# Kernel optimization log

Measured on AMD Instinct MI355X. Metric: run time of the kernel, lower is better.

## Reference

```python
import jax, jax.numpy as jnp
import numpy as np

B, L, H, NH = 8, 256, 128, 4
D = H // NH
NEG = jnp.float32(-(2.0 ** 32) + 1.0)


def setup_inputs() -> dict:
    key = jax.random.key(0)
    ks = jax.random.split(key, 12)
    f = lambda k, s, sc=1.0: jax.random.normal(k, s, dtype=jnp.float32) * sc
    inp = {
        "queries": f(ks[0], (B, L, H)),
        "keys": f(ks[1], (B, L, H)),
        "time_matrix_K": f(ks[2], (B, L, L, H), 0.05),
        "time_matrix_V": f(ks[3], (B, L, L, H), 0.05),
        "abs_pos_K": f(ks[4], (B, L, H), 0.1),
        "abs_pos_V": f(ks[5], (B, L, H), 0.1),
        "Wq": f(ks[6], (H, H), 1.0 / np.sqrt(H)),
        "bq": jnp.zeros((H,), jnp.float32),
        "Wk": f(ks[7], (H, H), 1.0 / np.sqrt(H)),
        "bk": jnp.zeros((H,), jnp.float32),
        "Wv": f(ks[8], (H, H), 1.0 / np.sqrt(H)),
        "bv": jnp.zeros((H,), jnp.float32),
        # True = padded query row (masked out)
        "time_mask": jax.random.uniform(ks[9], (B, L)) < 0.1,
        # causal mask: True above the diagonal = not attendable
        "attn_mask": jnp.triu(jnp.ones((L, L), dtype=bool), k=1),
    }
    return inp


def reference(queries, keys, time_matrix_K, time_matrix_V, abs_pos_K, abs_pos_V,
              Wq, bq, Wk, bk, Wv, bv, time_mask, attn_mask):
    # Linear projections (torch Linear: x @ W.T + b)
    Q = queries @ Wq.T + bq
    K = keys @ Wk.T + bk
    V = keys @ Wv.T + bv
    # head split: channels [i*D:(i+1)*D] -> head i  (equivalent to torch split/cat)
    Qh = Q.reshape(B, L, NH, D)
    Kh = K.reshape(B, L, NH, D)
    Vh = V.reshape(B, L, NH, D)
    pKh = abs_pos_K.reshape(B, L, NH, D)
    pVh = abs_pos_V.reshape(B, L, NH, D)
    tKh = time_matrix_K.reshape(B, L, L, NH, D)
    tVh = time_matrix_V.reshape(B, L, L, NH, D)
    # scores: QK^T + Q*absposK^T + per-row time-interval bias  -> [B,NH,L,L]
    aw = jnp.einsum('blhd,bmhd->bhlm', Qh, Kh)
    aw += jnp.einsum('blhd,bmhd->bhlm', Qh, pKh)
    aw += jnp.einsum('blmhd,blhd->bhlm', tKh, Qh)
    aw = aw * jnp.float32(1.0 / np.sqrt(D))
    mask = time_mask[:, None, :, None] | attn_mask[None, None, :, :]
    aw = jnp.where(mask, NEG, aw)
    A = jax.nn.softmax(aw, axis=-1)  # dropout omitted (eval mode)
    # outputs: A@V + A@absposV + per-row A @ time_matrix_V  -> [B,L,NH,D]
    out = jnp.einsum('bhlm,bmhd->blhd', A, Vh)
    out += jnp.einsum('bhlm,bmhd->blhd', A, pVh)
    out += jnp.einsum('bhlm,blmhd->blhd', A, tVh)
    return out.reshape(B, L, H)
```

## Files before the change

### kernel.cpp

```cpp
#include <hip/hip_runtime.h>
#include <math.h>

#define Bdim 8
#define Lq   256
#define Hd   128

static constexpr float kNEG = -4294967295.0f;
static constexpr float kScale = 0.17677669529663687f;
static constexpr float kUni = 0.00390625f;

typedef float f32x4 __attribute__((ext_vector_type(4)));

__device__ __forceinline__ f32x4 nt4(const float* p) {
    return __builtin_nontemporal_load((const f32x4*)p);
}

__global__ __launch_bounds__(256) void prep_kernel(
    const float* __restrict__ Wq, const float* __restrict__ Wk,
    const float* __restrict__ Wv, const unsigned char* __restrict__ raw,
    float* __restrict__ Wt, int* __restrict__ outmask)
{
    const int blk = blockIdx.x;
    if (blk < 12) {
        __shared__ float tile[64][65];
        const int mi = blk >> 2;
        const float* W = (mi == 0) ? Wq : (mi == 1) ? Wk : Wv;
        float* WT = Wt + mi * (Hd * Hd);
        const int ti = blk & 3;
        const int r0 = (ti >> 1) * 64, c0 = (ti & 1) * 64;
        #pragma unroll
        for (int k = 0; k < 16; ++k) {
            const int e = threadIdx.x + k * 256;
            const int r = e >> 6, c = e & 63;
            tile[r][c] = W[(r0 + r) * Hd + (c0 + c)];
        }
        __syncthreads();
        #pragma unroll
        for (int k = 0; k < 16; ++k) {
            const int e = threadIdx.x + k * 256;
            const int r = e >> 6, c = e & 63;
            WT[(c0 + r) * Hd + (r0 + c)] = tile[c][r];
        }
    } else {
        __shared__ int cnt;
        if (threadIdx.x == 0) cnt = 0;
        __syncthreads();
        const int n = Bdim * Lq;
        for (int i = threadIdx.x; i < n; i += 256)
            if ((i & 3) && raw[i]) atomicAdd(&cnt, 1);
        __syncthreads();
        const bool is_u8 = (cnt > 0);
        const int* raw32 = (const int*)raw;
        for (int i = threadIdx.x; i < n; i += 256) {
            const int v = is_u8 ? (int)raw[i] : raw32[i];
            outmask[i] = (v != 0) ? 1 : 0;
        }
    }
}

__global__ __launch_bounds__(512) void proj_kernel(
    const float* __restrict__ queries, const float* __restrict__ keys,
    const float* __restrict__ absK, const float* __restrict__ absV,
    const float* __restrict__ Wt,
    const float* __restrict__ bq, const float* __restrict__ bk,
    const float* __restrict__ bv,
    float* __restrict__ Qb, float* __restrict__ Kb, float* __restrict__ Vb)
{
    constexpr int R = 8;
    __shared__ float xq[R][Hd];
    __shared__ float xk[R][Hd];
    const int row0 = blockIdx.x * R;
    const int tid = threadIdx.x;
    #pragma unroll
    for (int k = 0; k < 2; ++k) {
        const int e = tid + k * 512;
        const int r = e >> 7, c = e & 127;
        xq[r][c] = queries[(row0 + r) * Hd + c];
        xk[r][c] = keys[(row0 + r) * Hd + c];
    }
    __syncthreads();

    const int o = tid & 127, rh = tid >> 7;
    const int r0 = rh * 2, r1 = rh * 2 + 1;
    const float* __restrict__ Wtq = Wt;
    const float* __restrict__ Wtk = Wt + Hd * Hd;
    const float* __restrict__ Wtv = Wt + 2 * Hd * Hd;

    float qa0 = bq[o], qa1 = qa0;
    float ka0 = bk[o] + absK[(row0 + r0) * Hd + o];
    float ka1 = bk[o] + absK[(row0 + r1) * Hd + o];
    float va0 = bv[o] + absV[(row0 + r0) * Hd + o];
    float va1 = bv[o] + absV[(row0 + r1) * Hd + o];

    #pragma unroll 4
    for (int i = 0; i < Hd; ++i) {
        const float wq = Wtq[i * Hd + o];
        const float wk = Wtk[i * Hd + o];
        const float wv = Wtv[i * Hd + o];
        const float x0 = xq[r0][i], x1 = xq[r1][i];
        const float y0 = xk[r0][i], y1 = xk[r1][i];
        qa0 += x0 * wq; qa1 += x1 * wq;
        ka0 += y0 * wk; ka1 += y1 * wk;
        va0 += y0 * wv; va1 += y1 * wv;
    }
    Qb[(row0 + r0) * Hd + o] = qa0;  Qb[(row0 + r1) * Hd + o] = qa1;
    Kb[(row0 + r0) * Hd + o] = ka0;  Kb[(row0 + r1) * Hd + o] = ka1;
    Vb[(row0 + r0) * Hd + o] = va0;  Vb[(row0 + r1) * Hd + o] = va1;
}

__global__ __launch_bounds__(256) void attn_kernel(
    const float* __restrict__ Qb, const float* __restrict__ Kb,
    const float* __restrict__ Vb,
    const float* __restrict__ tK, const float* __restrict__ tV,
    const int* __restrict__ tmask, float* __restrict__ out)
{
    const int bid = blockIdx.x;
    const int b  = bid & 7;
    const int hp = (bid >> 3) & 1;
    const int j  = bid >> 4;

    const int tid = threadIdx.x;
    const int w = tid >> 6;
    const int h = hp * 2 + (w & 1);
    const int p = j * 2 + (w >> 1);
    const int l0 = p;
    const int l1 = 255 - p;
    const int m_off = (tid >> 2) & 15;
    const int cg = tid & 3;
    const int ch = h * 32 + cg * 8;

    const float* q0b = Qb + ((size_t)b * Lq + l0) * Hd + ch;
    const float* q1b = Qb + ((size_t)b * Lq + l1) * Hd + ch;
    f32x4 q00 = *(const f32x4*)q0b, q01 = *(const f32x4*)(q0b + 4);
    f32x4 q10 = *(const f32x4*)q1b, q11 = *(const f32x4*)(q1b + 4);
    q00 *= kScale; q01 *= kScale; q10 *= kScale; q11 *= kScale;

    const bool mk0 = (tmask[b * Lq + l0] != 0);
    const bool mk1 = (tmask[b * Lq + l1] != 0);
    const int ntc0 = (l0 >> 4) + 1, ntc1 = (l1 >> 4) + 1;
    const int n10 = mk0 ? 0 : ntc0, n11 = mk1 ? 0 : ntc1;
    const int NT1 = (n10 > n11) ? n10 : n11;
    const int n20 = mk0 ? 16 : ntc0, n21 = mk1 ? 16 : ntc1;
    const int NT2 = (n20 > n21) ? n20 : n21;

    const float* kpt = Kb + (size_t)b * Lq * Hd + m_off * Hd + ch;
    const float* vpt = Vb + (size_t)b * Lq * Hd + m_off * Hd + ch;
    const float* t0p = tK + (((size_t)b * Lq + l0) * Lq + m_off) * Hd + ch;
    const float* t1p = tK + (((size_t)b * Lq + l1) * Lq + m_off) * Hd + ch;
    const float* u0p = tV + (((size_t)b * Lq + l0) * Lq + m_off) * Hd + ch;
    const float* u1p = tV + (((size_t)b * Lq + l1) * Lq + m_off) * Hd + ch;

    float s0[16], s1[16];
    #pragma unroll
    for (int t = 0; t < 16; ++t) { s0[t] = kNEG; s1[t] = kNEG; }

    #pragma unroll
    for (int t = 0; t < 16; ++t) {
        if (t < NT1) {
            const f32x4 ka = *(const f32x4*)(kpt + t * 2048);
            const f32x4 kb = *(const f32x4*)(kpt + t * 2048 + 4);
            const int m = t * 16 + m_off;
            if (t < n10) {
                const f32x4 sa = ka + nt4(t0p + t * 2048);
                const f32x4 sb = kb + nt4(t0p + t * 2048 + 4);
                float pp = q00.x*sa.x + q00.y*sa.y + q00.z*sa.z + q00.w*sa.w
                         + q01.x*sb.x + q01.y*sb.y + q01.z*sb.z + q01.w*sb.w;
                pp += __shfl_xor(pp, 1);
                pp += __shfl_xor(pp, 2);
                s0[t] = (m <= l0) ? pp : kNEG;
            }
            if (t < n11) {
                const f32x4 sa = ka + nt4(t1p + t * 2048);
                const f32x4 sb = kb + nt4(t1p + t * 2048 + 4);
                float pp = q10.x*sa.x + q10.y*sa.y + q10.z*sa.z + q10.w*sa.w
                         + q11.x*sb.x + q11.y*sb.y + q11.z*sb.z + q11.w*sb.w;
                pp += __shfl_xor(pp, 1);
                pp += __shfl_xor(pp, 2);
                s1[t] = (m <= l1) ? pp : kNEG;
            }
        }
    }

    if (!mk0) {
        float mx = s0[0];
        #pragma unroll
        for (int t = 1; t < 16; ++t) mx = fmaxf(mx, s0[t]);
        #pragma unroll
        for (int d = 4; d < 64; d <<= 1) mx = fmaxf(mx, __shfl_xor(mx, d));
        float sum = 0.f;
        #pragma unroll
        for (int t = 0; t < 16; ++t) { s0[t] = expf(s0[t] - mx); sum += s0[t]; }
        #pragma unroll
        for (int d = 4; d < 64; d <<= 1) sum += __shfl_xor(sum, d);
        const float inv = 1.0f / sum;
        #pragma unroll
        for (int t = 0; t < 16; ++t) s0[t] *= inv;
    } else {
        #pragma unroll
        for (int t = 0; t < 16; ++t) s0[t] = kUni;
    }
    if (!mk1) {
        float mx = s1[0];
        #pragma unroll
        for (int t = 1; t < 16; ++t) mx = fmaxf(mx, s1[t]);
        #pragma unroll
        for (int d = 4; d < 64; d <<= 1) mx = fmaxf(mx, __shfl_xor(mx, d));
        float sum = 0.f;
        #pragma unroll
        for (int t = 0; t < 16; ++t) { s1[t] = expf(s1[t] - mx); sum += s1[t]; }
        #pragma unroll
        for (int d = 4; d < 64; d <<= 1) sum += __shfl_xor(sum, d);
        const float inv = 1.0f / sum;
        #pragma unroll
        for (int t = 0; t < 16; ++t) s1[t] *= inv;
    } else {
        #pragma unroll
        for (int t = 0; t < 16; ++t) s1[t] = kUni;
    }

    f32x4 a00 = {0,0,0,0}, a01 = {0,0,0,0};
    f32x4 a10 = {0,0,0,0}, a11 = {0,0,0,0};
    #pragma unroll
    for (int t = 0; t < 16; ++t) {
        if (t < NT2) {
            const f32x4 va = *(const f32x4*)(vpt + t * 2048);
            const f32x4 vb = *(const f32x4*)(vpt + t * 2048 + 4);
            if (t < n20) {
                const f32x4 ta = nt4(u0p + t * 2048);
                const f32x4 tb = nt4(u0p + t * 2048 + 4);
                const float aw = s0[t];
                a00 += aw * (va + ta);
                a01 += aw * (vb + tb);
            }
            if (t < n21) {
                const f32x4 ta = nt4(u1p + t * 2048);
                const f32x4 tb = nt4(u1p + t * 2048 + 4);
                const float aw = s1[t];
                a10 += aw * (va + ta);
                a11 += aw * (vb + tb);
            }
        }
    }
    #pragma unroll
    for (int d = 4; d < 64; d <<= 1) {
        a00.x += __shfl_xor(a00.x, d); a00.y += __shfl_xor(a00.y, d);
        a00.z += __shfl_xor(a00.z, d); a00.w += __shfl_xor(a00.w, d);
        a01.x += __shfl_xor(a01.x, d); a01.y += __shfl_xor(a01.y, d);
        a01.z += __shfl_xor(a01.z, d); a01.w += __shfl_xor(a01.w, d);
        a10.x += __shfl_xor(a10.x, d); a10.y += __shfl_xor(a10.y, d);
        a10.z += __shfl_xor(a10.z, d); a10.w += __shfl_xor(a10.w, d);
        a11.x += __shfl_xor(a11.x, d); a11.y += __shfl_xor(a11.y, d);
        a11.z += __shfl_xor(a11.z, d); a11.w += __shfl_xor(a11.w, d);
    }
    if (m_off == 0) {
        float* o0 = out + ((size_t)b * Lq + l0) * Hd + ch;
        *(f32x4*)o0 = a00; *(f32x4*)(o0 + 4) = a01;
        float* o1 = out + ((size_t)b * Lq + l1) * Hd + ch;
        *(f32x4*)o1 = a10; *(f32x4*)(o1 + 4) = a11;
    }
}

extern "C" void kernel_launch(void* const* d_in, const int* in_sizes, int n_in,
                              void* d_out, int out_size, void* d_ws, size_t ws_size,
                              hipStream_t stream) {
    const float* queries = (const float*)d_in[0];
    const float* keys    = (const float*)d_in[1];
    const float* tK      = (const float*)d_in[2];
    const float* tV      = (const float*)d_in[3];
    const float* absK    = (const float*)d_in[4];
    const float* absV    = (const float*)d_in[5];
    const float* Wq      = (const float*)d_in[6];
    const float* bq      = (const float*)d_in[7];
    const float* Wk      = (const float*)d_in[8];
    const float* bk      = (const float*)d_in[9];
    const float* Wv      = (const float*)d_in[10];
    const float* bv      = (const float*)d_in[11];
    const unsigned char* tmask_raw = (const unsigned char*)d_in[12];

    float* outp = (float*)d_out;

    const int rows = Bdim * Lq;
    float* Qb = (float*)d_ws;
    float* Kb = Qb + (size_t)rows * Hd;
    float* Vb = Kb + (size_t)rows * Hd;
    int* tmask = (int*)(Vb + (size_t)rows * Hd);
    float* Wt = (float*)(tmask + rows);

    prep_kernel<<<13, 256, 0, stream>>>(Wq, Wk, Wv, tmask_raw, Wt, tmask);
    proj_kernel<<<rows / 8, 512, 0, stream>>>(queries, keys, absK, absV, Wt,
                                              bq, bk, bv, Qb, Kb, Vb);
    attn_kernel<<<1024, 256, 0, stream>>>(Qb, Kb, Vb, tK, tV, tmask, outp);
}
```

Baseline: 92.38 us.

## Split dense QK and AV products into separate kernels around time-matrix attention

Moves the Q·(K+absK) score term and the A·(V+absV) output term out of the streaming attention kernel into dedicated shared-memory qk and av kernels. The attention kernel now streams only the time matrices, reads precomputed scores, and writes the softmax weights to a workspace buffer. The av kernel reads those weights and adds its product into the output. Nontemporal loads are also replaced with plain loads. This cuts redundant K/V loads in the bandwidth-bound kernel, at the cost of two extra launches and extra score and weight traffic through global memory.

```diff
diff --git a/kernel.cpp b/kernel.cpp
--- a/kernel.cpp
+++ b/kernel.cpp
@@ -10,10 +10,6 @@
 static constexpr float kUni = 0.00390625f;
 
 typedef float f32x4 __attribute__((ext_vector_type(4)));
-
-__device__ __forceinline__ f32x4 nt4(const float* p) {
-    return __builtin_nontemporal_load((const f32x4*)p);
-}
 
 __global__ __launch_bounds__(256) void prep_kernel(
     const float* __restrict__ Wq, const float* __restrict__ Wk,
@@ -108,10 +104,86 @@
     Vb[(row0 + r0) * Hd + o] = va0;  Vb[(row0 + r1) * Hd + o] = va1;
 }
 
+__global__ __launch_bounds__(256) void qk_kernel(
+    const float* __restrict__ Qb, const float* __restrict__ Kb,
+    float* __restrict__ Sp)
+{
+    const int bid = blockIdx.x;
+    const int b = bid & 7, h = (bid >> 3) & 3, lt = bid >> 5;
+    const int lbase = lt * 32;
+    const int tid = threadIdx.x;
+
+    __shared__ float Qs[32][36];
+    #pragma unroll
+    for (int k = 0; k < 4; ++k) {
+        const int e = tid + k * 256;
+        Qs[e >> 5][e & 31] = Qb[(b * Lq + lbase + (e >> 5)) * Hd + h * 32 + (e & 31)];
+    }
+    f32x4 kr[8];
+    const float* kp = Kb + ((size_t)(b * Lq + tid)) * Hd + h * 32;
+    #pragma unroll
+    for (int g = 0; g < 8; ++g) kr[g] = *(const f32x4*)(kp + g * 4);
+    __syncthreads();
+
+    float* sprow = Sp + ((size_t)(b * 4 + h) * Lq + lbase) * Lq + tid;
+    #pragma unroll 4
+    for (int l = 0; l < 32; ++l) {
+        const f32x4* q4 = (const f32x4*)&Qs[l][0];
+        float s = 0.f;
+        #pragma unroll
+        for (int g = 0; g < 8; ++g) {
+            const f32x4 qv = q4[g];
+            s += qv.x * kr[g].x + qv.y * kr[g].y
+               + qv.z * kr[g].z + qv.w * kr[g].w;
+        }
+        sprow[(size_t)l * Lq] = s * kScale;
+    }
+}
+
+__global__ __launch_bounds__(256) void av_kernel(
+    const float* __restrict__ A, const float* __restrict__ Vb,
+    float* __restrict__ out)
+{
+    const int bid = blockIdx.x;
+    const int b = bid & 7, h = (bid >> 3) & 3, lt = bid >> 5;
+    const int lbase = lt * 32;
+    const int tid = threadIdx.x;
+
+    __shared__ float As[32][260];
+    __shared__ float Vs[256][32];
+
+    const float* Abase = A + ((size_t)(b * 4 + h) * Lq + lbase) * Lq;
+    #pragma unroll
+    for (int k = 0; k < 32; ++k) {
+        const int e = tid + k * 256;
+        As[e >> 8][e & 255] = Abase[(size_t)(e >> 8) * Lq + (e & 255)];
+    }
+    #pragma unroll
+    for (int k = 0; k < 32; ++k) {
+        const int e = tid + k * 256;
+        Vs[e >> 5][e & 31] = Vb[((size_t)(b * Lq + (e >> 5))) * Hd + h * 32 + (e & 31)];
+    }
+    __syncthreads();
+
+    const int l = tid >> 3, d4 = tid & 7;
+    f32x4 acc = {0, 0, 0, 0};
+    #pragma unroll 4
+    for (int mb = 0; mb < 64; ++mb) {
+        const f32x4 a4 = *(const f32x4*)&As[l][mb * 4];
+        acc += a4.x * *(const f32x4*)&Vs[mb * 4 + 0][d4 * 4];
+        acc += a4.y * *(const f32x4*)&Vs[mb * 4 + 1][d4 * 4];
+        acc += a4.z * *(const f32x4*)&Vs[mb * 4 + 2][d4 * 4];
+        acc += a4.w * *(const f32x4*)&Vs[mb * 4 + 3][d4 * 4];
+    }
+    float* op = out + ((size_t)(b * Lq + lbase + l)) * Hd + h * 32 + d4 * 4;
+    const f32x4 cur = *(const f32x4*)op;
+    *(f32x4*)op = cur + acc;
+}
+
 __global__ __launch_bounds__(256) void attn_kernel(
-    const float* __restrict__ Qb, const float* __restrict__ Kb,
-    const float* __restrict__ Vb,
+    const float* __restrict__ Qb,
     const float* __restrict__ tK, const float* __restrict__ tV,
+    const float* __restrict__ Sp, float* __restrict__ Aout,
     const int* __restrict__ tmask, float* __restrict__ out)
 {
     const int bid = blockIdx.x;
@@ -139,45 +211,43 @@
     const bool mk1 = (tmask[b * Lq + l1] != 0);
     const int ntc0 = (l0 >> 4) + 1, ntc1 = (l1 >> 4) + 1;
     const int n10 = mk0 ? 0 : ntc0, n11 = mk1 ? 0 : ntc1;
-    const int NT1 = (n10 > n11) ? n10 : n11;
     const int n20 = mk0 ? 16 : ntc0, n21 = mk1 ? 16 : ntc1;
-    const int NT2 = (n20 > n21) ? n20 : n21;
-
-    const float* kpt = Kb + (size_t)b * Lq * Hd + m_off * Hd + ch;
-    const float* vpt = Vb + (size_t)b * Lq * Hd + m_off * Hd + ch;
+
     const float* t0p = tK + (((size_t)b * Lq + l0) * Lq + m_off) * Hd + ch;
     const float* t1p = tK + (((size_t)b * Lq + l1) * Lq + m_off) * Hd + ch;
     const float* u0p = tV + (((size_t)b * Lq + l0) * Lq + m_off) * Hd + ch;
     const float* u1p = tV + (((size_t)b * Lq + l1) * Lq + m_off) * Hd + ch;
 
+    const size_t abase = (size_t)(b * 4 + h) * Lq * Lq;
+    const float* sp0 = Sp + abase + (size_t)l0 * Lq;
+    const float* sp1 = Sp + abase + (size_t)l1 * Lq;
+
     float s0[16], s1[16];
     #pragma unroll
     for (int t = 0; t < 16; ++t) { s0[t] = kNEG; s1[t] = kNEG; }
 
     #pragma unroll
     for (int t = 0; t < 16; ++t) {
-        if (t < NT1) {
-            const f32x4 ka = *(const f32x4*)(kpt + t * 2048);
-            const f32x4 kb = *(const f32x4*)(kpt + t * 2048 + 4);
-            const int m = t * 16 + m_off;
-            if (t < n10) {
-                const f32x4 sa = ka + nt4(t0p + t * 2048);
-                const f32x4 sb = kb + nt4(t0p + t * 2048 + 4);
-                float pp = q00.x*sa.x + q00.y*sa.y + q00.z*sa.z + q00.w*sa.w
-                         + q01.x*sb.x + q01.y*sb.y + q01.z*sb.z + q01.w*sb.w;
-                pp += __shfl_xor(pp, 1);
-                pp += __shfl_xor(pp, 2);
-                s0[t] = (m <= l0) ? pp : kNEG;
-            }
-            if (t < n11) {
-                const f32x4 sa = ka + nt4(t1p + t * 2048);
-                const f32x4 sb = kb + nt4(t1p + t * 2048 + 4);
-                float pp = q10.x*sa.x + q10.y*sa.y + q10.z*sa.z + q10.w*sa.w
-                         + q11.x*sb.x + q11.y*sb.y + q11.z*sb.z + q11.w*sb.w;
-                pp += __shfl_xor(pp, 1);
-                pp += __shfl_xor(pp, 2);
-                s1[t] = (m <= l1) ? pp : kNEG;
-            }
+        const int m = t * 16 + m_off;
+        if (t < n10) {
+            const f32x4 ta = *(const f32x4*)(t0p + t * 2048);
+            const f32x4 tb = *(const f32x4*)(t0p + t * 2048 + 4);
+            const float sp = sp0[m];
+            float pp = q00.x*ta.x + q00.y*ta.y + q00.z*ta.z + q00.w*ta.w
+                     + q01.x*tb.x + q01.y*tb.y + q01.z*tb.z + q01.w*tb.w;
+            pp += __shfl_xor(pp, 1);
+            pp += __shfl_xor(pp, 2);
+            s0[t] = (m <= l0) ? (pp + sp) : kNEG;
+        }
+        if (t < n11) {
+            const f32x4 ta = *(const f32x4*)(t1p + t * 2048);
+            const f32x4 tb = *(const f32x4*)(t1p + t * 2048 + 4);
+            const float sp = sp1[m];
+            float pp = q10.x*ta.x + q10.y*ta.y + q10.z*ta.z + q10.w*ta.w
+                     + q11.x*tb.x + q11.y*tb.y + q11.z*tb.z + q11.w*tb.w;
+            pp += __shfl_xor(pp, 1);
+            pp += __shfl_xor(pp, 2);
+            s1[t] = (m <= l1) ? (pp + sp) : kNEG;
         }
     }
 
@@ -218,27 +288,31 @@
         for (int t = 0; t < 16; ++t) s1[t] = kUni;
     }
 
+    if (cg == 0) {
+        float* a0r = Aout + abase + (size_t)l0 * Lq + m_off;
+        float* a1r = Aout + abase + (size_t)l1 * Lq + m_off;
+        #pragma unroll
+        for (int t = 0; t < 16; ++t) {
+            a0r[t * 16] = s0[t];
+            a1r[t * 16] = s1[t];
+        }
+    }
+
     f32x4 a00 = {0,0,0,0}, a01 = {0,0,0,0};
     f32x4 a10 = {0,0,0,0}, a11 = {0,0,0,0};
     #pragma unroll
     for (int t = 0; t < 16; ++t) {
-        if (t < NT2) {
-            const f32x4 va = *(const f32x4*)(vpt + t * 2048);
-            const f32x4 vb = *(const f32x4*)(vpt + t * 2048 + 4);
-            if (t < n20) {
-                const f32x4 ta = nt4(u0p + t * 2048);
-                const f32x4 tb = nt4(u0p + t * 2048 + 4);
-                const float aw = s0[t];
-                a00 += aw * (va + ta);
-                a01 += aw * (vb + tb);
-            }
-            if (t < n21) {
-                const f32x4 ta = nt4(u1p + t * 2048);
-                const f32x4 tb = nt4(u1p + t * 2048 + 4);
-                const float aw = s1[t];
-                a10 += aw * (va + ta);
-                a11 += aw * (vb + tb);
-            }
+        if (t < n20) {
+            const f32x4 ta = *(const f32x4*)(u0p + t * 2048);
+            const f32x4 tb = *(const f32x4*)(u0p + t * 2048 + 4);
+            a00 += s0[t] * ta;
+            a01 += s0[t] * tb;
+        }
+        if (t < n21) {
+            const f32x4 ta = *(const f32x4*)(u1p + t * 2048);
+            const f32x4 tb = *(const f32x4*)(u1p + t * 2048 + 4);
+            a10 += s1[t] * ta;
+            a11 += s1[t] * tb;
         }
     }
     #pragma unroll
@@ -285,9 +359,13 @@
     float* Vb = Kb + (size_t)rows * Hd;
     int* tmask = (int*)(Vb + (size_t)rows * Hd);
     float* Wt = (float*)(tmask + rows);
+    float* Sp = Wt + 3 * Hd * Hd;
+    float* Aw = Sp + (size_t)32 * Lq * Lq;
 
     prep_kernel<<<13, 256, 0, stream>>>(Wq, Wk, Wv, tmask_raw, Wt, tmask);
     proj_kernel<<<rows / 8, 512, 0, stream>>>(queries, keys, absK, absV, Wt,
                                               bq, bk, bv, Qb, Kb, Vb);
-    attn_kernel<<<1024, 256, 0, stream>>>(Qb, Kb, Vb, tK, tV, tmask, outp);
-}
+    qk_kernel<<<256, 256, 0, stream>>>(Qb, Kb, Sp);
+    attn_kernel<<<1024, 256, 0, stream>>>(Qb, tK, tV, Sp, Aw, tmask, outp);
+    av_kernel<<<256, 256, 0, stream>>>(Aw, Vb, outp);
+}
```

After: 100.5 us. +8.8%, slower.

## Process four query rows per wave to reuse K/V loads, drop nontemporal loads

Applied to the files above, without the earlier changes.

Each wave now handles one head and four query rows (p, 127-p, 128+p, 255-p) rather than two rows with head pairs split across waves. K and V tiles are loaded once and reused across four rows, and the balanced row choice evens out causal work. The grid shrinks from 1024 to 512 blocks. Loads of the time matrices switch from nontemporal to ordinary loads. This raises register pressure and lowers the number of waves in flight, which may reduce latency hiding on the memory-bound time-matrix streams.

```diff
diff --git a/kernel.cpp b/kernel.cpp
--- a/kernel.cpp
+++ b/kernel.cpp
@@ -10,10 +10,6 @@
 static constexpr float kUni = 0.00390625f;
 
 typedef float f32x4 __attribute__((ext_vector_type(4)));
-
-__device__ __forceinline__ f32x4 nt4(const float* p) {
-    return __builtin_nontemporal_load((const f32x4*)p);
-}
 
 __global__ __launch_bounds__(256) void prep_kernel(
     const float* __restrict__ Wq, const float* __restrict__ Wk,
@@ -115,44 +111,45 @@
     const int* __restrict__ tmask, float* __restrict__ out)
 {
     const int bid = blockIdx.x;
-    const int b  = bid & 7;
-    const int hp = (bid >> 3) & 1;
-    const int j  = bid >> 4;
-
+    const int b = bid & 7;
+    const int p = bid >> 3;
     const int tid = threadIdx.x;
-    const int w = tid >> 6;
-    const int h = hp * 2 + (w & 1);
-    const int p = j * 2 + (w >> 1);
-    const int l0 = p;
-    const int l1 = 255 - p;
-    const int m_off = (tid >> 2) & 15;
-    const int cg = tid & 3;
+    const int h = tid >> 6;
+    const int lane = tid & 63;
+    const int m_off = (lane >> 2) & 15;
+    const int cg = lane & 3;
     const int ch = h * 32 + cg * 8;
 
-    const float* q0b = Qb + ((size_t)b * Lq + l0) * Hd + ch;
-    const float* q1b = Qb + ((size_t)b * Lq + l1) * Hd + ch;
-    f32x4 q00 = *(const f32x4*)q0b, q01 = *(const f32x4*)(q0b + 4);
-    f32x4 q10 = *(const f32x4*)q1b, q11 = *(const f32x4*)(q1b + 4);
-    q00 *= kScale; q01 *= kScale; q10 *= kScale; q11 *= kScale;
-
-    const bool mk0 = (tmask[b * Lq + l0] != 0);
-    const bool mk1 = (tmask[b * Lq + l1] != 0);
-    const int ntc0 = (l0 >> 4) + 1, ntc1 = (l1 >> 4) + 1;
-    const int n10 = mk0 ? 0 : ntc0, n11 = mk1 ? 0 : ntc1;
-    const int NT1 = (n10 > n11) ? n10 : n11;
-    const int n20 = mk0 ? 16 : ntc0, n21 = mk1 ? 16 : ntc1;
-    const int NT2 = (n20 > n21) ? n20 : n21;
-
-    const float* kpt = Kb + (size_t)b * Lq * Hd + m_off * Hd + ch;
-    const float* vpt = Vb + (size_t)b * Lq * Hd + m_off * Hd + ch;
-    const float* t0p = tK + (((size_t)b * Lq + l0) * Lq + m_off) * Hd + ch;
-    const float* t1p = tK + (((size_t)b * Lq + l1) * Lq + m_off) * Hd + ch;
-    const float* u0p = tV + (((size_t)b * Lq + l0) * Lq + m_off) * Hd + ch;
-    const float* u1p = tV + (((size_t)b * Lq + l1) * Lq + m_off) * Hd + ch;
-
-    float s0[16], s1[16];
-    #pragma unroll
-    for (int t = 0; t < 16; ++t) { s0[t] = kNEG; s1[t] = kNEG; }
+    const int ls[4] = {p, 127 - p, 128 + p, 255 - p};
+
+    f32x4 q[4][2];
+    const float* tKp[4];
+    const float* tVp[4];
+    bool  mk[4];
+    int   n1[4], n2[4];
+    int NT1 = 0, NT2 = 0;
+    #pragma unroll
+    for (int i = 0; i < 4; ++i) {
+        const size_t row = ((size_t)b * Lq + ls[i]) * Hd;
+        q[i][0] = *(const f32x4*)(Qb + row + ch) * kScale;
+        q[i][1] = *(const f32x4*)(Qb + row + ch + 4) * kScale;
+        tKp[i] = tK + row * Lq + (size_t)m_off * Hd + ch;
+        tVp[i] = tV + row * Lq + (size_t)m_off * Hd + ch;
+        mk[i] = (tmask[b * Lq + ls[i]] != 0);
+        const int nt = (ls[i] >> 4) + 1;
+        n1[i] = mk[i] ? 0 : nt;
+        n2[i] = mk[i] ? 16 : nt;
+        NT1 = (n1[i] > NT1) ? n1[i] : NT1;
+        NT2 = (n2[i] > NT2) ? n2[i] : NT2;
+    }
+    const float* kpt = Kb + (size_t)b * Lq * Hd + (size_t)m_off * Hd + ch;
+    const float* vpt = Vb + (size_t)b * Lq * Hd + (size_t)m_off * Hd + ch;
+
+    float s[4][16];
+    #pragma unroll
+    for (int i = 0; i < 4; ++i)
+        #pragma unroll
+        for (int t = 0; t < 16; ++t) s[i][t] = kNEG;
 
     #pragma unroll
     for (int t = 0; t < 16; ++t) {
@@ -160,103 +157,86 @@
             const f32x4 ka = *(const f32x4*)(kpt + t * 2048);
             const f32x4 kb = *(const f32x4*)(kpt + t * 2048 + 4);
             const int m = t * 16 + m_off;
-            if (t < n10) {
-                const f32x4 sa = ka + nt4(t0p + t * 2048);
-                const f32x4 sb = kb + nt4(t0p + t * 2048 + 4);
-                float pp = q00.x*sa.x + q00.y*sa.y + q00.z*sa.z + q00.w*sa.w
-                         + q01.x*sb.x + q01.y*sb.y + q01.z*sb.z + q01.w*sb.w;
-                pp += __shfl_xor(pp, 1);
-                pp += __shfl_xor(pp, 2);
-                s0[t] = (m <= l0) ? pp : kNEG;
+            #pragma unroll
+            for (int i = 0; i < 4; ++i) {
+                if (t < n1[i]) {
+                    const f32x4 sa = ka + *(const f32x4*)(tKp[i] + t * 2048);
+                    const f32x4 sb = kb + *(const f32x4*)(tKp[i] + t * 2048 + 4);
+                    float pp = q[i][0].x*sa.x + q[i][0].y*sa.y
+                             + q[i][0].z*sa.z + q[i][0].w*sa.w
+                             + q[i][1].x*sb.x + q[i][1].y*sb.y
+                             + q[i][1].z*sb.z + q[i][1].w*sb.w;
+                    pp += __shfl_xor(pp, 1);
+                    pp += __shfl_xor(pp, 2);
+                    s[i][t] = (m <= ls[i]) ? pp : kNEG;
+                }
             }
-            if (t < n11) {
-                const f32x4 sa = ka + nt4(t1p + t * 2048);
-                const f32x4 sb = kb + nt4(t1p + t * 2048 + 4);
-                float pp = q10.x*sa.x + q10.y*sa.y + q10.z*sa.z + q10.w*sa.w
-                         + q11.x*sb.x + q11.y*sb.y + q11.z*sb.z + q11.w*sb.w;
-                pp += __shfl_xor(pp, 1);
-                pp += __shfl_xor(pp, 2);
-                s1[t] = (m <= l1) ? pp : kNEG;
-            }
-        }
-    }
-
-    if (!mk0) {
-        float mx = s0[0];
-        #pragma unroll
-        for (int t = 1; t < 16; ++t) mx = fmaxf(mx, s0[t]);
-        #pragma unroll
-        for (int d = 4; d < 64; d <<= 1) mx = fmaxf(mx, __shfl_xor(mx, d));
-        float sum = 0.f;
-        #pragma unroll
-        for (int t = 0; t < 16; ++t) { s0[t] = expf(s0[t] - mx); sum += s0[t]; }
-        #pragma unroll
-        for (int d = 4; d < 64; d <<= 1) sum += __shfl_xor(sum, d);
-        const float inv = 1.0f / sum;
-        #pragma unroll
-        for (int t = 0; t < 16; ++t) s0[t] *= inv;
-    } else {
-        #pragma unroll
-        for (int t = 0; t < 16; ++t) s0[t] = kUni;
-    }
-    if (!mk1) {
-        float mx = s1[0];
-        #pragma unroll
-        for (int t = 1; t < 16; ++t) mx = fmaxf(mx, s1[t]);
-        #pragma unroll
-        for (int d = 4; d < 64; d <<= 1) mx = fmaxf(mx, __shfl_xor(mx, d));
-        float sum = 0.f;
-        #pragma unroll
-        for (int t = 0; t < 16; ++t) { s1[t] = expf(s1[t] - mx); sum += s1[t]; }
-        #pragma unroll
-        for (int d = 4; d < 64; d <<= 1) sum += __shfl_xor(sum, d);
-        const float inv = 1.0f / sum;
-        #pragma unroll
-        for (int t = 0; t < 16; ++t) s1[t] *= inv;
-    } else {
-        #pragma unroll
-        for (int t = 0; t < 16; ++t) s1[t] = kUni;
-    }
-
-    f32x4 a00 = {0,0,0,0}, a01 = {0,0,0,0};
-    f32x4 a10 = {0,0,0,0}, a11 = {0,0,0,0};
+        }
+    }
+
+    #pragma unroll
+    for (int i = 0; i < 4; ++i) {
+        if (!mk[i]) {
+            float mx = s[i][0];
+            #pragma unroll
+            for (int t = 1; t < 16; ++t) mx = fmaxf(mx, s[i][t]);
+            #pragma unroll
+            for (int d = 4; d < 64; d <<= 1) mx = fmaxf(mx, __shfl_xor(mx, d));
+            float sum = 0.f;
+            #pragma unroll
+            for (int t = 0; t < 16; ++t) { s[i][t] = expf(s[i][t] - mx); sum += s[i][t]; }
+            #pragma unroll
+            for (int d = 4; d < 64; d <<= 1) sum += __shfl_xor(sum, d);
+            const float inv = 1.0f / sum;
+            #pragma unroll
+            for (int t = 0; t < 16; ++t) s[i][t] *= inv;
+        } else {
+            #pragma unroll
+            for (int t = 0; t < 16; ++t) s[i][t] = kUni;
+        }
+    }
+
+    f32x4 acc[4][2];
+    #pragma unroll
+    for (int i = 0; i < 4; ++i) { acc[i][0] = (f32x4){0,0,0,0}; acc[i][1] = (f32x4){0,0,0,0}; }
+
     #pragma unroll
     for (int t = 0; t < 16; ++t) {
         if (t < NT2) {
             const f32x4 va = *(const f32x4*)(vpt + t * 2048);
             const f32x4 vb = *(const f32x4*)(vpt + t * 2048 + 4);
-            if (t < n20) {
-                const f32x4 ta = nt4(u0p + t * 2048);
-                const f32x4 tb = nt4(u0p + t * 2048 + 4);
-                const float aw = s0[t];
-                a00 += aw * (va + ta);
-                a01 += aw * (vb + tb);
+            #pragma unroll
+            for (int i = 0; i < 4; ++i) {
+                if (t < n2[i]) {
+                    const f32x4 ta = *(const f32x4*)(tVp[i] + t * 2048);
+                    const f32x4 tb = *(const f32x4*)(tVp[i] + t * 2048 + 4);
+                    acc[i][0] += s[i][t] * (va + ta);
+                    acc[i][1] += s[i][t] * (vb + tb);
+                }
             }
-            if (t < n21) {
-                const f32x4 ta = nt4(u1p + t * 2048);
-                const f32x4 tb = nt4(u1p + t * 2048 + 4);
-                const float aw = s1[t];
-                a10 += aw * (va + ta);
-                a11 += aw * (vb + tb);
-            }
-        }
-    }
-    #pragma unroll
-    for (int d = 4; d < 64; d <<= 1) {
-        a00.x += __shfl_xor(a00.x, d); a00.y += __shfl_xor(a00.y, d);
-        a00.z += __shfl_xor(a00.z, d); a00.w += __shfl_xor(a00.w, d);
-        a01.x += __shfl_xor(a01.x, d); a01.y += __shfl_xor(a01.y, d);
-        a01.z += __shfl_xor(a01.z, d); a01.w += __shfl_xor(a01.w, d);
-        a10.x += __shfl_xor(a10.x, d); a10.y += __shfl_xor(a10.y, d);
-        a10.z += __shfl_xor(a10.z, d); a10.w += __shfl_xor(a10.w, d);
-        a11.x += __shfl_xor(a11.x, d); a11.y += __shfl_xor(a11.y, d);
-        a11.z += __shfl_xor(a11.z, d); a11.w += __shfl_xor(a11.w, d);
+        }
+    }
+    #pragma unroll
+    for (int i = 0; i < 4; ++i) {
+        #pragma unroll
+        for (int d = 4; d < 64; d <<= 1) {
+            acc[i][0].x += __shfl_xor(acc[i][0].x, d);
+            acc[i][0].y += __shfl_xor(acc[i][0].y, d);
+            acc[i][0].z += __shfl_xor(acc[i][0].z, d);
+            acc[i][0].w += __shfl_xor(acc[i][0].w, d);
+            acc[i][1].x += __shfl_xor(acc[i][1].x, d);
+            acc[i][1].y += __shfl_xor(acc[i][1].y, d);
+            acc[i][1].z += __shfl_xor(acc[i][1].z, d);
+            acc[i][1].w += __shfl_xor(acc[i][1].w, d);
+        }
     }
     if (m_off == 0) {
-        float* o0 = out + ((size_t)b * Lq + l0) * Hd + ch;
-        *(f32x4*)o0 = a00; *(f32x4*)(o0 + 4) = a01;
-        float* o1 = out + ((size_t)b * Lq + l1) * Hd + ch;
-        *(f32x4*)o1 = a10; *(f32x4*)(o1 + 4) = a11;
+        #pragma unroll
+        for (int i = 0; i < 4; ++i) {
+            float* o = out + ((size_t)b * Lq + ls[i]) * Hd + ch;
+            *(f32x4*)o       = acc[i][0];
+            *(f32x4*)(o + 4) = acc[i][1];
+        }
     }
 }
 
@@ -289,5 +269,5 @@
     prep_kernel<<<13, 256, 0, stream>>>(Wq, Wk, Wv, tmask_raw, Wt, tmask);
     proj_kernel<<<rows / 8, 512, 0, stream>>>(queries, keys, absK, absV, Wt,
                                               bq, bk, bv, Qb, Kb, Vb);
-    attn_kernel<<<1024, 256, 0, stream>>>(Qb, Kb, Vb, tK, tV, tmask, outp);
-}
+    attn_kernel<<<512, 256, 0, stream>>>(Qb, Kb, Vb, tK, tV, tmask, outp);
+}
```

Measured after the change: 89.61 us. 3.0% less time.

## Drop prep kernel, widen per-lane channel tiles, read weights row-wise

Applied to the files above, without the earlier changes.

Removes the separate prep kernel: the weight transpose is replaced by per-thread contiguous row reads of W with vector loads, and the mask dtype detection moves into the attention kernel via a wave ballot. In the attention kernel each lane now covers 16 channels across 32 key positions instead of 8 channels across 16, halving the tile count and the shuffle reduction depth. Nontemporal loads on the time matrices are replaced by ordinary loads, and launch bounds request 4 blocks per CU. The risks are higher register pressure from the wider per-lane vectors and uncoalesced strided weight reads in the projection.

```diff
diff --git a/kernel.cpp b/kernel.cpp
--- a/kernel.cpp
+++ b/kernel.cpp
@@ -11,57 +11,11 @@
 
 typedef float f32x4 __attribute__((ext_vector_type(4)));
 
-__device__ __forceinline__ f32x4 nt4(const float* p) {
-    return __builtin_nontemporal_load((const f32x4*)p);
-}
-
-__global__ __launch_bounds__(256) void prep_kernel(
-    const float* __restrict__ Wq, const float* __restrict__ Wk,
-    const float* __restrict__ Wv, const unsigned char* __restrict__ raw,
-    float* __restrict__ Wt, int* __restrict__ outmask)
-{
-    const int blk = blockIdx.x;
-    if (blk < 12) {
-        __shared__ float tile[64][65];
-        const int mi = blk >> 2;
-        const float* W = (mi == 0) ? Wq : (mi == 1) ? Wk : Wv;
-        float* WT = Wt + mi * (Hd * Hd);
-        const int ti = blk & 3;
-        const int r0 = (ti >> 1) * 64, c0 = (ti & 1) * 64;
-        #pragma unroll
-        for (int k = 0; k < 16; ++k) {
-            const int e = threadIdx.x + k * 256;
-            const int r = e >> 6, c = e & 63;
-            tile[r][c] = W[(r0 + r) * Hd + (c0 + c)];
-        }
-        __syncthreads();
-        #pragma unroll
-        for (int k = 0; k < 16; ++k) {
-            const int e = threadIdx.x + k * 256;
-            const int r = e >> 6, c = e & 63;
-            WT[(c0 + r) * Hd + (r0 + c)] = tile[c][r];
-        }
-    } else {
-        __shared__ int cnt;
-        if (threadIdx.x == 0) cnt = 0;
-        __syncthreads();
-        const int n = Bdim * Lq;
-        for (int i = threadIdx.x; i < n; i += 256)
-            if ((i & 3) && raw[i]) atomicAdd(&cnt, 1);
-        __syncthreads();
-        const bool is_u8 = (cnt > 0);
-        const int* raw32 = (const int*)raw;
-        for (int i = threadIdx.x; i < n; i += 256) {
-            const int v = is_u8 ? (int)raw[i] : raw32[i];
-            outmask[i] = (v != 0) ? 1 : 0;
-        }
-    }
-}
-
 __global__ __launch_bounds__(512) void proj_kernel(
     const float* __restrict__ queries, const float* __restrict__ keys,
     const float* __restrict__ absK, const float* __restrict__ absV,
-    const float* __restrict__ Wt,
+    const float* __restrict__ Wq, const float* __restrict__ Wk,
+    const float* __restrict__ Wv,
     const float* __restrict__ bq, const float* __restrict__ bk,
     const float* __restrict__ bv,
     float* __restrict__ Qb, float* __restrict__ Kb, float* __restrict__ Vb)
@@ -82,9 +36,9 @@
 
     const int o = tid & 127, rh = tid >> 7;
     const int r0 = rh * 2, r1 = rh * 2 + 1;
-    const float* __restrict__ Wtq = Wt;
-    const float* __restrict__ Wtk = Wt + Hd * Hd;
-    const float* __restrict__ Wtv = Wt + 2 * Hd * Hd;
+    const float* __restrict__ wqr = Wq + o * Hd;
+    const float* __restrict__ wkr = Wk + o * Hd;
+    const float* __restrict__ wvr = Wv + o * Hd;
 
     float qa0 = bq[o], qa1 = qa0;
     float ka0 = bk[o] + absK[(row0 + r0) * Hd + o];
@@ -93,26 +47,30 @@
     float va1 = bv[o] + absV[(row0 + r1) * Hd + o];
 
     #pragma unroll 4
-    for (int i = 0; i < Hd; ++i) {
-        const float wq = Wtq[i * Hd + o];
-        const float wk = Wtk[i * Hd + o];
-        const float wv = Wtv[i * Hd + o];
-        const float x0 = xq[r0][i], x1 = xq[r1][i];
-        const float y0 = xk[r0][i], y1 = xk[r1][i];
-        qa0 += x0 * wq; qa1 += x1 * wq;
-        ka0 += y0 * wk; ka1 += y1 * wk;
-        va0 += y0 * wv; va1 += y1 * wv;
+    for (int i4 = 0; i4 < 32; ++i4) {
+        const f32x4 wq4 = *(const f32x4*)(wqr + i4 * 4);
+        const f32x4 wk4 = *(const f32x4*)(wkr + i4 * 4);
+        const f32x4 wv4 = *(const f32x4*)(wvr + i4 * 4);
+        #pragma unroll
+        for (int k = 0; k < 4; ++k) {
+            const int i = i4 * 4 + k;
+            const float x0 = xq[r0][i], x1 = xq[r1][i];
+            const float y0 = xk[r0][i], y1 = xk[r1][i];
+            qa0 += x0 * wq4[k]; qa1 += x1 * wq4[k];
+            ka0 += y0 * wk4[k]; ka1 += y1 * wk4[k];
+            va0 += y0 * wv4[k]; va1 += y1 * wv4[k];
+        }
     }
     Qb[(row0 + r0) * Hd + o] = qa0;  Qb[(row0 + r1) * Hd + o] = qa1;
     Kb[(row0 + r0) * Hd + o] = ka0;  Kb[(row0 + r1) * Hd + o] = ka1;
     Vb[(row0 + r0) * Hd + o] = va0;  Vb[(row0 + r1) * Hd + o] = va1;
 }
 
-__global__ __launch_bounds__(256) void attn_kernel(
+__global__ __launch_bounds__(256, 4) void attn_kernel(
     const float* __restrict__ Qb, const float* __restrict__ Kb,
     const float* __restrict__ Vb,
     const float* __restrict__ tK, const float* __restrict__ tV,
-    const int* __restrict__ tmask, float* __restrict__ out)
+    const unsigned char* __restrict__ mraw, float* __restrict__ out)
 {
     const int bid = blockIdx.x;
     const int b  = bid & 7;
@@ -121,61 +79,80 @@
 
     const int tid = threadIdx.x;
     const int w = tid >> 6;
+    const int lane = tid & 63;
     const int h = hp * 2 + (w & 1);
     const int p = j * 2 + (w >> 1);
     const int l0 = p;
     const int l1 = 255 - p;
-    const int m_off = (tid >> 2) & 15;
-    const int cg = tid & 3;
-    const int ch = h * 32 + cg * 8;
+    const int half = lane & 1;
+    const int mo = lane >> 1;
+    const int ch = h * 32 + half * 16;
+
+    bool is_u8;
+    {
+        const unsigned int* r32 = (const unsigned int*)mraw;
+        unsigned int acc = 0;
+        #pragma unroll
+        for (int k = 0; k < 8; ++k) acc |= r32[lane + k * 64] & 0xFFFFFF00u;
+        is_u8 = (__ballot(acc != 0) != 0);
+    }
+    const int mi0 = b * Lq + l0, mi1 = b * Lq + l1;
+    const bool mk0 = is_u8 ? (mraw[mi0] != 0) : (((const int*)mraw)[mi0] != 0);
+    const bool mk1 = is_u8 ? (mraw[mi1] != 0) : (((const int*)mraw)[mi1] != 0);
 
     const float* q0b = Qb + ((size_t)b * Lq + l0) * Hd + ch;
     const float* q1b = Qb + ((size_t)b * Lq + l1) * Hd + ch;
-    f32x4 q00 = *(const f32x4*)q0b, q01 = *(const f32x4*)(q0b + 4);
-    f32x4 q10 = *(const f32x4*)q1b, q11 = *(const f32x4*)(q1b + 4);
-    q00 *= kScale; q01 *= kScale; q10 *= kScale; q11 *= kScale;
-
-    const bool mk0 = (tmask[b * Lq + l0] != 0);
-    const bool mk1 = (tmask[b * Lq + l1] != 0);
-    const int ntc0 = (l0 >> 4) + 1, ntc1 = (l1 >> 4) + 1;
+    f32x4 q0[4], q1[4];
+    #pragma unroll
+    for (int g = 0; g < 4; ++g) {
+        q0[g] = *(const f32x4*)(q0b + g * 4) * kScale;
+        q1[g] = *(const f32x4*)(q1b + g * 4) * kScale;
+    }
+
+    const int ntc0 = (l0 >> 5) + 1, ntc1 = (l1 >> 5) + 1;
     const int n10 = mk0 ? 0 : ntc0, n11 = mk1 ? 0 : ntc1;
     const int NT1 = (n10 > n11) ? n10 : n11;
-    const int n20 = mk0 ? 16 : ntc0, n21 = mk1 ? 16 : ntc1;
-    const int NT2 = (n20 > n21) ? n20 : n21;
-
-    const float* kpt = Kb + (size_t)b * Lq * Hd + m_off * Hd + ch;
-    const float* vpt = Vb + (size_t)b * Lq * Hd + m_off * Hd + ch;
-    const float* t0p = tK + (((size_t)b * Lq + l0) * Lq + m_off) * Hd + ch;
-    const float* t1p = tK + (((size_t)b * Lq + l1) * Lq + m_off) * Hd + ch;
-    const float* u0p = tV + (((size_t)b * Lq + l0) * Lq + m_off) * Hd + ch;
-    const float* u1p = tV + (((size_t)b * Lq + l1) * Lq + m_off) * Hd + ch;
-
-    float s0[16], s1[16];
-    #pragma unroll
-    for (int t = 0; t < 16; ++t) { s0[t] = kNEG; s1[t] = kNEG; }
-
-    #pragma unroll
-    for (int t = 0; t < 16; ++t) {
+    const int n20 = mk0 ? 8 : ntc0, n21 = mk1 ? 8 : ntc1;
+
+    const float* kpt = Kb + (size_t)b * Lq * Hd + (size_t)mo * Hd + ch;
+    const float* vpt = Vb + (size_t)b * Lq * Hd + (size_t)mo * Hd + ch;
+    const float* t0p = tK + (((size_t)b * Lq + l0) * Lq + mo) * Hd + ch;
+    const float* t1p = tK + (((size_t)b * Lq + l1) * Lq + mo) * Hd + ch;
+    const float* u0p = tV + (((size_t)b * Lq + l0) * Lq + mo) * Hd + ch;
+    const float* u1p = tV + (((size_t)b * Lq + l1) * Lq + mo) * Hd + ch;
+
+    float s0[8], s1[8];
+    #pragma unroll
+    for (int t = 0; t < 8; ++t) { s0[t] = kNEG; s1[t] = kNEG; }
+
+    #pragma unroll
+    for (int t = 0; t < 8; ++t) {
         if (t < NT1) {
-            const f32x4 ka = *(const f32x4*)(kpt + t * 2048);
-            const f32x4 kb = *(const f32x4*)(kpt + t * 2048 + 4);
-            const int m = t * 16 + m_off;
+            f32x4 kk[4];
+            #pragma unroll
+            for (int g = 0; g < 4; ++g)
+                kk[g] = *(const f32x4*)(kpt + t * 4096 + g * 4);
+            const int m = t * 32 + mo;
             if (t < n10) {
-                const f32x4 sa = ka + nt4(t0p + t * 2048);
-                const f32x4 sb = kb + nt4(t0p + t * 2048 + 4);
-                float pp = q00.x*sa.x + q00.y*sa.y + q00.z*sa.z + q00.w*sa.w
-                         + q01.x*sb.x + q01.y*sb.y + q01.z*sb.z + q01.w*sb.w;
+                float pp = 0.f;
+                #pragma unroll
+                for (int g = 0; g < 4; ++g) {
+                    const f32x4 sa = kk[g] + *(const f32x4*)(t0p + t * 4096 + g * 4);
+                    pp += q0[g].x * sa.x + q0[g].y * sa.y
+                        + q0[g].z * sa.z + q0[g].w * sa.w;
+                }
                 pp += __shfl_xor(pp, 1);
-                pp += __shfl_xor(pp, 2);
                 s0[t] = (m <= l0) ? pp : kNEG;
             }
             if (t < n11) {
-                const f32x4 sa = ka + nt4(t1p + t * 2048);
-                const f32x4 sb = kb + nt4(t1p + t * 2048 + 4);
-                float pp = q10.x*sa.x + q10.y*sa.y + q10.z*sa.z + q10.w*sa.w
-                         + q11.x*sb.x + q11.y*sb.y + q11.z*sb.z + q11.w*sb.w;
+                float pp = 0.f;
+                #pragma unroll
+                for (int g = 0; g < 4; ++g) {
+                    const f32x4 sa = kk[g] + *(const f32x4*)(t1p + t * 4096 + g * 4);
+                    pp += q1[g].x * sa.x + q1[g].y * sa.y
+                        + q1[g].z * sa.z + q1[g].w * sa.w;
+                }
                 pp += __shfl_xor(pp, 1);
-                pp += __shfl_xor(pp, 2);
                 s1[t] = (m <= l1) ? pp : kNEG;
             }
         }
@@ -184,79 +161,82 @@
     if (!mk0) {
         float mx = s0[0];
         #pragma unroll
-        for (int t = 1; t < 16; ++t) mx = fmaxf(mx, s0[t]);
-        #pragma unroll
-        for (int d = 4; d < 64; d <<= 1) mx = fmaxf(mx, __shfl_xor(mx, d));
+        for (int t = 1; t < 8; ++t) mx = fmaxf(mx, s0[t]);
+        #pragma unroll
+        for (int d = 2; d < 64; d <<= 1) mx = fmaxf(mx, __shfl_xor(mx, d));
         float sum = 0.f;
         #pragma unroll
-        for (int t = 0; t < 16; ++t) { s0[t] = expf(s0[t] - mx); sum += s0[t]; }
-        #pragma unroll
-        for (int d = 4; d < 64; d <<= 1) sum += __shfl_xor(sum, d);
+        for (int t = 0; t < 8; ++t) { s0[t] = expf(s0[t] - mx); sum += s0[t]; }
+        #pragma unroll
+        for (int d = 2; d < 64; d <<= 1) sum += __shfl_xor(sum, d);
         const float inv = 1.0f / sum;
         #pragma unroll
-        for (int t = 0; t < 16; ++t) s0[t] *= inv;
+        for (int t = 0; t < 8; ++t) s0[t] *= inv;
     } else {
         #pragma unroll
-        for (int t = 0; t < 16; ++t) s0[t] = kUni;
+        for (int t = 0; t < 8; ++t) s0[t] = kUni;
     }
     if (!mk1) {
         float mx = s1[0];
         #pragma unroll
-        for (int t = 1; t < 16; ++t) mx = fmaxf(mx, s1[t]);
-        #pragma unroll
-        for (int d = 4; d < 64; d <<= 1) mx = fmaxf(mx, __shfl_xor(mx, d));
+        for (int t = 1; t < 8; ++t) mx = fmaxf(mx, s1[t]);
+        #pragma unroll
+        for (int d = 2; d < 64; d <<= 1) mx = fmaxf(mx, __shfl_xor(mx, d));
         float sum = 0.f;
         #pragma unroll
-        for (int t = 0; t < 16; ++t) { s1[t] = expf(s1[t] - mx); sum += s1[t]; }
-        #pragma unroll
-        for (int d = 4; d < 64; d <<= 1) sum += __shfl_xor(sum, d);
+        for (int t = 0; t < 8; ++t) { s1[t] = expf(s1[t] - mx); sum += s1[t]; }
+        #pragma unroll
+        for (int d = 2; d < 64; d <<= 1) sum += __shfl_xor(sum, d);
         const float inv = 1.0f / sum;
         #pragma unroll
-        for (int t = 0; t < 16; ++t) s1[t] *= inv;
+        for (int t = 0; t < 8; ++t) s1[t] *= inv;
     } else {
         #pragma unroll
-        for (int t = 0; t < 16; ++t) s1[t] = kUni;
-    }
-
-    f32x4 a00 = {0,0,0,0}, a01 = {0,0,0,0};
-    f32x4 a10 = {0,0,0,0}, a11 = {0,0,0,0};
-    #pragma unroll
-    for (int t = 0; t < 16; ++t) {
+        for (int t = 0; t < 8; ++t) s1[t] = kUni;
+    }
+
+    f32x4 a0[4] = {{0,0,0,0},{0,0,0,0},{0,0,0,0},{0,0,0,0}};
+    f32x4 a1[4] = {{0,0,0,0},{0,0,0,0},{0,0,0,0},{0,0,0,0}};
+    const int NT2 = (n20 > n21) ? n20 : n21;
+    #pragma unroll
+    for (int t = 0; t < 8; ++t) {
         if (t < NT2) {
-            const f32x4 va = *(const f32x4*)(vpt + t * 2048);
-            const f32x4 vb = *(const f32x4*)(vpt + t * 2048 + 4);
+            f32x4 vv[4];
+            #pragma unroll
+            for (int g = 0; g < 4; ++g)
+                vv[g] = *(const f32x4*)(vpt + t * 4096 + g * 4);
             if (t < n20) {
-                const f32x4 ta = nt4(u0p + t * 2048);
-                const f32x4 tb = nt4(u0p + t * 2048 + 4);
                 const float aw = s0[t];
-                a00 += aw * (va + ta);
-                a01 += aw * (vb + tb);
+                #pragma unroll
+                for (int g = 0; g < 4; ++g)
+                    a0[g] += aw * (vv[g] + *(const f32x4*)(u0p + t * 4096 + g * 4));
             }
             if (t < n21) {
-                const f32x4 ta = nt4(u1p + t * 2048);
-                const f32x4 tb = nt4(u1p + t * 2048 + 4);
                 const float aw = s1[t];
-                a10 += aw * (va + ta);
-                a11 += aw * (vb + tb);
-            }
-        }
-    }
-    #pragma unroll
-    for (int d = 4; d < 64; d <<= 1) {
-        a00.x += __shfl_xor(a00.x, d); a00.y += __shfl_xor(a00.y, d);
-        a00.z += __shfl_xor(a00.z, d); a00.w += __shfl_xor(a00.w, d);
-        a01.x += __shfl_xor(a01.x, d); a01.y += __shfl_xor(a01.y, d);
-        a01.z += __shfl_xor(a01.z, d); a01.w += __shfl_xor(a01.w, d);
-        a10.x += __shfl_xor(a10.x, d); a10.y += __shfl_xor(a10.y, d);
-        a10.z += __shfl_xor(a10.z, d); a10.w += __shfl_xor(a10.w, d);
-        a11.x += __shfl_xor(a11.x, d); a11.y += __shfl_xor(a11.y, d);
-        a11.z += __shfl_xor(a11.z, d); a11.w += __shfl_xor(a11.w, d);
-    }
-    if (m_off == 0) {
+                #pragma unroll
+                for (int g = 0; g < 4; ++g)
+                    a1[g] += aw * (vv[g] + *(const f32x4*)(u1p + t * 4096 + g * 4));
+            }
+        }
+    }
+    #pragma unroll
+    for (int d = 2; d < 64; d <<= 1) {
+        #pragma unroll
+        for (int g = 0; g < 4; ++g) {
+            a0[g].x += __shfl_xor(a0[g].x, d); a0[g].y += __shfl_xor(a0[g].y, d);
+            a0[g].z += __shfl_xor(a0[g].z, d); a0[g].w += __shfl_xor(a0[g].w, d);
+            a1[g].x += __shfl_xor(a1[g].x, d); a1[g].y += __shfl_xor(a1[g].y, d);
+            a1[g].z += __shfl_xor(a1[g].z, d); a1[g].w += __shfl_xor(a1[g].w, d);
+        }
+    }
+    if (mo == 0) {
         float* o0 = out + ((size_t)b * Lq + l0) * Hd + ch;
-        *(f32x4*)o0 = a00; *(f32x4*)(o0 + 4) = a01;
         float* o1 = out + ((size_t)b * Lq + l1) * Hd + ch;
-        *(f32x4*)o1 = a10; *(f32x4*)(o1 + 4) = a11;
+        #pragma unroll
+        for (int g = 0; g < 4; ++g) {
+            *(f32x4*)(o0 + g * 4) = a0[g];
+            *(f32x4*)(o1 + g * 4) = a1[g];
+        }
     }
 }
 
@@ -283,11 +263,9 @@
     float* Qb = (float*)d_ws;
     float* Kb = Qb + (size_t)rows * Hd;
     float* Vb = Kb + (size_t)rows * Hd;
-    int* tmask = (int*)(Vb + (size_t)rows * Hd);
-    float* Wt = (float*)(tmask + rows);
-
-    prep_kernel<<<13, 256, 0, stream>>>(Wq, Wk, Wv, tmask_raw, Wt, tmask);
-    proj_kernel<<<rows / 8, 512, 0, stream>>>(queries, keys, absK, absV, Wt,
-                                              bq, bk, bv, Qb, Kb, Vb);
-    attn_kernel<<<1024, 256, 0, stream>>>(Qb, Kb, Vb, tK, tV, tmask, outp);
+
+    proj_kernel<<<rows / 8, 512, 0, stream>>>(queries, keys, absK, absV,
+                                              Wq, Wk, Wv, bq, bk, bv,
+                                              Qb, Kb, Vb);
+    attn_kernel<<<1024, 256, 0, stream>>>(Qb, Kb, Vb, tK, tV, tmask_raw, outp);
 }
```

Result: slower. 104.2 us (+12.8%).
